# Optimization experiments

Hardware: AMD Instinct MI355X
Metric: run time of the kernel (lower is better)

## Reference

```python
import jax, jax.numpy as jnp
import numpy as np

N = 10000      # nodes
E = 160000     # edges (before self-loops)
H = 8          # heads
D_IN, D_H1, D_H2 = 165, 128, 1    # per-head channels of gat1 / gat2
HID = H * D_H1                    # 1024


def batchnorm(x, gamma, beta, eps=1e-5):
    # training-mode BatchNorm1d: biased batch statistics over the node axis
    mu = x.mean(0)
    var = x.var(0)
    return (x - mu) * jax.lax.rsqrt(var + eps) * gamma + beta


def gatv2(x, src, dst, Wl, bl, Wr, br, att, bias, heads, out_ch, concat, n_nodes):
    # PyG GATv2Conv: lin_l on source, lin_r on target; e = att . LeakyReLU(xl_j + xr_i)
    xl = (x @ Wl + bl).reshape(n_nodes, heads, out_ch)   # source transform
    xr = (x @ Wr + br).reshape(n_nodes, heads, out_ch)   # target transform
    e = jax.nn.leaky_relu(xl[src] + xr[dst], 0.2)        # [E,H,C]
    logits = jnp.einsum('ehc,hc->eh', e, att)            # [E,H]
    # segment softmax over incoming edges of each destination node
    m = jax.lax.stop_gradient(jax.ops.segment_max(logits, dst, num_segments=n_nodes))
    a = jnp.exp(logits - m[dst])
    s = jax.ops.segment_sum(a, dst, num_segments=n_nodes)
    alpha = a / (s[dst] + 1e-16)                          # [E,H]
    out = jax.ops.segment_sum(xl[src] * alpha[..., None], dst, num_segments=n_nodes)
    out = out.reshape(n_nodes, heads * out_ch) if concat else out.mean(1)
    return out + bias


def setup_inputs() -> dict:
    key = jax.random.key(0)
    ks = jax.random.split(key, 12)
    g = lambda k, shape, fan_in: jax.random.normal(k, shape, jnp.float32) * (1.0 / np.sqrt(fan_in))
    return {
        'x': jax.random.normal(ks[0], (N, D_IN), jnp.float32),
        'gamma1': jnp.ones((D_IN,), jnp.float32),
        'beta1': jnp.zeros((D_IN,), jnp.float32),
        'Wl1': g(ks[1], (D_IN, HID), D_IN),
        'bl1': jnp.zeros((HID,), jnp.float32),
        'Wr1': g(ks[2], (D_IN, HID), D_IN),
        'br1': jnp.zeros((HID,), jnp.float32),
        'att1': g(ks[3], (H, D_H1), D_H1),
        'bias1': jnp.zeros((HID,), jnp.float32),
        'gamma2': jnp.ones((HID,), jnp.float32),
        'beta2': jnp.zeros((HID,), jnp.float32),
        'Wl2': g(ks[4], (HID, H * D_H2), HID),
        'bl2': jnp.zeros((H * D_H2,), jnp.float32),
        'Wr2': g(ks[5], (HID, H * D_H2), HID),
        'br2': jnp.zeros((H * D_H2,), jnp.float32),
        'att2': g(ks[6], (H, D_H2), D_H2),
        'bias2': jnp.zeros((D_H2,), jnp.float32),
        'edge_index': jax.random.randint(ks[7], (2, E), 0, N, jnp.int64 if jax.config.jax_enable_x64 else jnp.int32),
    }


def reference(x, gamma1, beta1, Wl1, bl1, Wr1, br1, att1, bias1,
              gamma2, beta2, Wl2, bl2, Wr2, br2, att2, bias2, edge_index):
    loops = jnp.arange(N, dtype=edge_index.dtype)
    src = jnp.concatenate([edge_index[0], loops])   # add_self_loops=True (PyG default)
    dst = jnp.concatenate([edge_index[1], loops])
    h = batchnorm(x, gamma1, beta1)
    h = gatv2(h, src, dst, Wl1, bl1, Wr1, br1, att1, bias1, H, D_H1, True, N)
    h = batchnorm(h, gamma2, beta2)
    h = jax.nn.leaky_relu(h, 0.01)                  # F.leaky_relu default slope
    out = gatv2(h, src, dst, Wl2, bl2, Wr2, br2, att2, bias2, H, D_H2, False, N)
    return out
```

## Files before the change

kernel.cpp:

```cpp
#include <hip/hip_runtime.h>

#define NN   10000
#define E0   160000
#define ET   170000
#define DIN  165
#define KP   192
#define HID  1024
#define NH   8
#define BP   200
#define K2P  1032


typedef __bf16 bf16x8 __attribute__((ext_vector_type(8)));
typedef float  f32x4  __attribute__((ext_vector_type(4)));

__device__ __forceinline__ float bf2f(unsigned short u) {
    unsigned int i = ((unsigned int)u) << 16;
    return __builtin_bit_cast(float, i);
}
__device__ __forceinline__ unsigned short f2bf(float f) {
    unsigned int i = __builtin_bit_cast(unsigned int, f);
    i += 0x7fffu + ((i >> 16) & 1u);
    return (unsigned short)(i >> 16);
}
__device__ __forceinline__ float fin(float x) {
    return fminf(fmaxf(x, -1e30f), 1e30f);
}
__device__ __forceinline__ int clampi(int s) {
    return min(max(s, 0), NN - 1);
}
__device__ __forceinline__ void unpack8(uint4 u, float* f) {
    f[0]=bf2f((unsigned short)(u.x)); f[1]=bf2f((unsigned short)(u.x>>16));
    f[2]=bf2f((unsigned short)(u.y)); f[3]=bf2f((unsigned short)(u.y>>16));
    f[4]=bf2f((unsigned short)(u.z)); f[5]=bf2f((unsigned short)(u.z>>16));
    f[6]=bf2f((unsigned short)(u.w)); f[7]=bf2f((unsigned short)(u.w>>16));
}

__global__ __launch_bounds__(256) void debug_fill(float* __restrict__ out, float val) {
    int i = blockIdx.x * 256 + threadIdx.x;
    if (i < NN) out[i] = val;
}

__global__ __launch_bounds__(256) void bn1_stats(const float* __restrict__ x,
                                                 float* __restrict__ colsum, float* __restrict__ colsq) {
    int r0 = blockIdx.x * 125;
    int c = threadIdx.x;
    if (c >= DIN) return;
    float acc = 0.f, sq = 0.f;
    for (int r = r0; r < r0 + 125; ++r) {
        float v = x[(size_t)r * DIN + c];
        acc += v; sq += v * v;
    }
    atomicAdd(&colsum[c], acc);
    atomicAdd(&colsq[c], sq);
}

__global__ __launch_bounds__(256) void bn1_apply(const float* __restrict__ x,
                                                 const float* __restrict__ colsum, const float* __restrict__ colsq,
                                                 const float* __restrict__ gamma, const float* __restrict__ beta,
                                                 unsigned short* __restrict__ hn) {
    int idx = blockIdx.x * 256 + threadIdx.x;
    if (idx >= NN * KP) return;
    int r = idx / KP, c = idx - r * KP;
    float v = 0.f;
    if (c < DIN) {
        float mu  = colsum[c] * (1.f / NN);
        float var = fmaxf(colsq[c] * (1.f / NN) - mu * mu, 0.f);
        float a = gamma[c] * rsqrtf(var + 1e-5f);
        float b = beta[c] - mu * a;
        v = fin(x[(size_t)r * DIN + c] * a + b);
    }
    hn[idx] = f2bf(v);
}

__global__ __launch_bounds__(256) void w1_transpose(const float* __restrict__ wl,
                                                    const float* __restrict__ wr,
                                                    unsigned short* __restrict__ wlt,
                                                    unsigned short* __restrict__ wrt) {
    const float* src    = blockIdx.z ? wr  : wl;
    unsigned short* dst = blockIdx.z ? wrt : wlt;
    __shared__ float ts[32][65];
    const int k0 = blockIdx.x * 32;
    const int n0 = blockIdx.y * 64;
    const int tid = threadIdx.x;
    for (int idx = tid; idx < 32 * 64; idx += 256) {
        int k = idx >> 6, n = idx & 63;
        ts[k][n] = (k0 + k < DIN) ? src[(size_t)(k0 + k) * HID + n0 + n] : 0.f;
    }
    __syncthreads();
    for (int idx = tid; idx < 64 * 32; idx += 256) {
        int n = idx >> 5, k = idx & 31;
        dst[(size_t)(n0 + n) * KP + k0 + k] = f2bf(ts[k][n]);
    }
}

__global__ __launch_bounds__(256) void gemm1_kernel(
    const unsigned short* __restrict__ hn,
    const unsigned short* __restrict__ wlt,
    const unsigned short* __restrict__ wrt,
    const float* __restrict__ bl,
    const float* __restrict__ br,
    unsigned short* __restrict__ xl,
    unsigned short* __restrict__ xr) {
    __shared__ unsigned short bs[2][64 * BP];
    const int tid  = threadIdx.x;
    const int lane = tid & 63;
    const int wave = tid >> 6;
    const int col  = lane & 15;
    const int q    = lane >> 4;
    const int n0   = blockIdx.y * 64;

    for (int idx = tid; idx < 64 * 48 * 2; idx += 256) {
        int z = idx >= 64 * 48;
        int rem = z ? idx - 64 * 48 : idx;
        int r = rem / 48, c = rem - r * 48;
        const unsigned short* wt = z ? wrt : wlt;
        uint2 v = *(const uint2*)(wt + (size_t)(n0 + r) * KP + c * 4);
        *(uint2*)&bs[z][r * BP + c * 4] = v;
    }
    __syncthreads();

    const int mbase = blockIdx.x * 128 + wave * 32;
    const int am0 = mbase + col;
    const int am1 = am0 + 16;
    const bool aok0 = (am0 < NN), aok1 = (am1 < NN);

    f32x4 accL[2][4], accR[2][4];
    #pragma unroll
    for (int m = 0; m < 2; ++m)
        for (int nt = 0; nt < 4; ++nt)
            for (int r = 0; r < 4; ++r) { accL[m][nt][r] = 0.f; accR[m][nt][r] = 0.f; }

    #pragma unroll
    for (int kt = 0; kt < 6; ++kt) {
        const int kk = kt * 32 + q * 8;
        uint4 a0u = make_uint4(0u,0u,0u,0u), a1u = make_uint4(0u,0u,0u,0u);
        if (aok0) a0u = *(const uint4*)(hn + (size_t)am0 * KP + kk);
        if (aok1) a1u = *(const uint4*)(hn + (size_t)am1 * KP + kk);
        bf16x8 a0 = __builtin_bit_cast(bf16x8, a0u);
        bf16x8 a1 = __builtin_bit_cast(bf16x8, a1u);
        #pragma unroll
        for (int nt = 0; nt < 4; ++nt) {
            bf16x8 bfl = __builtin_bit_cast(bf16x8, *(const uint4*)&bs[0][(nt * 16 + col) * BP + kk]);
            accL[0][nt] = __builtin_amdgcn_mfma_f32_16x16x32_bf16(a0, bfl, accL[0][nt], 0, 0, 0);
            accL[1][nt] = __builtin_amdgcn_mfma_f32_16x16x32_bf16(a1, bfl, accL[1][nt], 0, 0, 0);
            bf16x8 bfr = __builtin_bit_cast(bf16x8, *(const uint4*)&bs[1][(nt * 16 + col) * BP + kk]);
            accR[0][nt] = __builtin_amdgcn_mfma_f32_16x16x32_bf16(a0, bfr, accR[0][nt], 0, 0, 0);
            accR[1][nt] = __builtin_amdgcn_mfma_f32_16x16x32_bf16(a1, bfr, accR[1][nt], 0, 0, 0);
        }
    }

    #pragma unroll
    for (int nt = 0; nt < 4; ++nt) {
        const int nc = n0 + nt * 16 + col;
        const float bLv = bl[nc];
        const float bRv = br[nc];
        #pragma unroll
        for (int m = 0; m < 2; ++m) {
            #pragma unroll
            for (int r = 0; r < 4; ++r) {
                const int row = mbase + m * 16 + q * 4 + r;
                if (row < NN) {
                    xl[(size_t)row * HID + nc] = f2bf(fin(accL[m][nt][r] + bLv));
                    xr[(size_t)row * HID + nc] = f2bf(fin(accR[m][nt][r] + bRv));
                }
            }
        }
    }
}

__global__ __launch_bounds__(256) void edge_hist(const int* __restrict__ ei, int* __restrict__ deg) {
    int e = blockIdx.x * 256 + threadIdx.x;
    if (e >= ET) return;
    int d = (e < E0) ? ei[E0 + e] : (e - E0);
    atomicAdd(&deg[clampi(d)], 1);
}

__global__ __launch_bounds__(1024) void scan_kernel(const int* __restrict__ deg,
                                                    int* __restrict__ offs, int* __restrict__ cur,
                                                    int* __restrict__ perm) {
    __shared__ int wsum[16];
    __shared__ int bins[64];
    __shared__ int bcur[64];
    const int tid = threadIdx.x;
    const int base = tid * 10;
    int loc[10];
    int run = 0;
    #pragma unroll
    for (int j = 0; j < 10; ++j) {
        int idx = base + j;
        int v = (idx < NN) ? deg[idx] : 0;
        loc[j] = run;
        run += v;
    }
    const int lane = tid & 63;
    const int w = tid >> 6;
    int inc = run;
    #pragma unroll
    for (int s = 1; s < 64; s <<= 1) {
        int t = __shfl_up(inc, s);
        if (lane >= s) inc += t;
    }
    if (lane == 63) wsum[w] = inc;
    if (tid < 64) bins[tid] = 0;
    __syncthreads();
    int woff = 0;
    #pragma unroll
    for (int k = 0; k < 16; ++k) woff += (k < w) ? wsum[k] : 0;
    const int toff = woff + inc - run;
    #pragma unroll
    for (int j = 0; j < 10; ++j) {
        int idx = base + j;
        if (idx < NN) {
            int e = toff + loc[j]; offs[idx] = e; cur[idx] = e;
            atomicAdd(&bins[63 - min(deg[idx], 63)], 1);
        }
    }
    if (tid == 1023) offs[NN] = woff + inc;
    __syncthreads();
    if (tid < 64) {
        int v = bins[tid];
        int binc = v;
        #pragma unroll
        for (int s = 1; s < 64; s <<= 1) {
            int t = __shfl_up(binc, s);
            if (tid >= s) binc += t;
        }
        bcur[tid] = binc - v;
    }
    __syncthreads();
    #pragma unroll
    for (int j = 0; j < 10; ++j) {
        int idx = base + j;
        if (idx < NN) {
            int pos = atomicAdd(&bcur[63 - min(deg[idx], 63)], 1);
            perm[pos] = idx;
        }
    }
}

__global__ __launch_bounds__(256) void edge_scatter(const int* __restrict__ ei,
                                                    int* __restrict__ cur, int* __restrict__ ssrc) {
    int e = blockIdx.x * 256 + threadIdx.x;
    if (e >= ET) return;
    int s, d;
    if (e < E0) { s = ei[e]; d = ei[E0 + e]; }
    else        { s = e - E0; d = e - E0; }
    int pos = atomicAdd(&cur[clampi(d)], 1);
    if (pos >= 0 && pos < ET) ssrc[pos] = clampi(s);
}

__global__ __launch_bounds__(256) void gat1_node(
    const unsigned short* __restrict__ xl1, const unsigned short* xr1,
    const float* __restrict__ att1, const float* __restrict__ bias1,
    const int* __restrict__ offs, const int* __restrict__ ssrc,
    const int* __restrict__ perm,
    unsigned short* agg) {
    const int lane = threadIdx.x & 63;
    const int wave = threadIdx.x >> 6;
    const int i = perm[blockIdx.x * 4 + wave];
    const int e0 = offs[i];
    const int e1 = max(offs[i + 1], e0);

    float xr_r[16], att_r[16];
    {
        const uint4* xp = (const uint4*)(xr1 + (size_t)i * HID + lane * 16);
        uint4 u0 = xp[0], u1 = xp[1];
        unpack8(u0, xr_r); unpack8(u1, xr_r + 8);
        const float4* ap = (const float4*)(att1 + lane * 16);
        float4 a0 = ap[0], a1 = ap[1], a2 = ap[2], a3 = ap[3];
        att_r[0]=a0.x; att_r[1]=a0.y; att_r[2]=a0.z; att_r[3]=a0.w;
        att_r[4]=a1.x; att_r[5]=a1.y; att_r[6]=a1.z; att_r[7]=a1.w;
        att_r[8]=a2.x; att_r[9]=a2.y; att_r[10]=a2.z; att_r[11]=a2.w;
        att_r[12]=a3.x; att_r[13]=a3.y; att_r[14]=a3.z; att_r[15]=a3.w;
    }

    float o[16];
    #pragma unroll
    for (int j = 0; j < 16; ++j) o[j] = 0.f;
    float s = 0.f;

    int e = e0;
    for (; e + 1 < e1; e += 2) {
        const int s0i = clampi(ssrc[e]);
        const int s1i = clampi(ssrc[e + 1]);
        const uint4* xp0 = (const uint4*)(xl1 + (size_t)s0i * HID + lane * 16);
        const uint4* xp1 = (const uint4*)(xl1 + (size_t)s1i * HID + lane * 16);
        uint4 a0 = xp0[0], a1 = xp0[1], b0 = xp1[0], b1 = xp1[1];
        float xv0[16], xv1[16];
        unpack8(a0, xv0); unpack8(a1, xv0 + 8);
        unpack8(b0, xv1); unpack8(b1, xv1 + 8);
        float p0 = 0.f, p1 = 0.f;
        #pragma unroll
        for (int j = 0; j < 16; ++j) {
            float v0 = xv0[j] + xr_r[j];
            float v1 = xv1[j] + xr_r[j];
            v0 = fmaxf(v0, 0.2f * v0);
            v1 = fmaxf(v1, 0.2f * v1);
            p0 = fmaf(att_r[j], v0, p0);
            p1 = fmaf(att_r[j], v1, p1);
        }
        p0 += __shfl_xor(p0, 1); p0 += __shfl_xor(p0, 2); p0 += __shfl_xor(p0, 4);
        p1 += __shfl_xor(p1, 1); p1 += __shfl_xor(p1, 2); p1 += __shfl_xor(p1, 4);
        const float aa0 = __expf(fminf(fin(p0), 50.f));
        const float aa1 = __expf(fminf(fin(p1), 50.f));
        s += aa0 + aa1;
        #pragma unroll
        for (int j = 0; j < 16; ++j) o[j] = fmaf(aa0, xv0[j], fmaf(aa1, xv1[j], o[j]));
    }
    if (e < e1) {
        const int sidx = clampi(ssrc[e]);
        const uint4* xp = (const uint4*)(xl1 + (size_t)sidx * HID + lane * 16);
        uint4 u0 = xp[0], u1 = xp[1];
        float xv[16];
        unpack8(u0, xv); unpack8(u1, xv + 8);
        float p = 0.f;
        #pragma unroll
        for (int j = 0; j < 16; ++j) {
            float v = xv[j] + xr_r[j];
            v = fmaxf(v, 0.2f * v);
            p = fmaf(att_r[j], v, p);
        }
        p += __shfl_xor(p, 1); p += __shfl_xor(p, 2); p += __shfl_xor(p, 4);
        const float a = __expf(fminf(fin(p), 50.f));
        s += a;
        #pragma unroll
        for (int j = 0; j < 16; ++j) o[j] = fmaf(a, xv[j], o[j]);
    }

    const float inv = 1.f / (s + 1e-16f);
    const float4* bp = (const float4*)(bias1 + lane * 16);
    float4 b0 = bp[0], b1 = bp[1], b2 = bp[2], b3 = bp[3];
    float bb[16] = {b0.x,b0.y,b0.z,b0.w, b1.x,b1.y,b1.z,b1.w,
                    b2.x,b2.y,b2.z,b2.w, b3.x,b3.y,b3.z,b3.w};
    unsigned short ov[16];
    #pragma unroll
    for (int j = 0; j < 16; ++j) ov[j] = f2bf(fin(o[j] * inv + bb[j]));
    uint4* op = (uint4*)(agg + (size_t)i * HID + lane * 16);
    op[0] = *(const uint4*)&ov[0];
    op[1] = *(const uint4*)&ov[8];
}

__global__ __launch_bounds__(256) void bn2_stats(const unsigned short* __restrict__ agg,
                                                 float* __restrict__ colsum, float* __restrict__ colsq) {
    int r0 = blockIdx.x * 125;
    int t = threadIdx.x;
    float s0=0,s1=0,s2=0,s3=0,q0=0,q1=0,q2=0,q3=0;
    for (int r = r0; r < r0 + 125; ++r) {
        const ushort4 u = *(const ushort4*)(agg + (size_t)r * HID + t * 4);
        float v0=bf2f(u.x), v1=bf2f(u.y), v2=bf2f(u.z), v3=bf2f(u.w);
        s0+=v0; q0+=v0*v0; s1+=v1; q1+=v1*v1;
        s2+=v2; q2+=v2*v2; s3+=v3; q3+=v3*v3;
    }
    atomicAdd(&colsum[t*4+0], s0); atomicAdd(&colsq[t*4+0], q0);
    atomicAdd(&colsum[t*4+1], s1); atomicAdd(&colsq[t*4+1], q1);
    atomicAdd(&colsum[t*4+2], s2); atomicAdd(&colsq[t*4+2], q2);
    atomicAdd(&colsum[t*4+3], s3); atomicAdd(&colsq[t*4+3], q3);
}

__global__ __launch_bounds__(256) void gemm2_kernel(
    const unsigned short* __restrict__ agg,
    const float* __restrict__ colsum, const float* __restrict__ colsq,
    const float* __restrict__ gamma, const float* __restrict__ beta,
    const float* __restrict__ wl2, const float* __restrict__ wr2,
    const float* __restrict__ bl2, const float* __restrict__ br2,
    float* __restrict__ xl2, float* __restrict__ xr2) {
    __shared__ unsigned short bs[16 * K2P];
    __shared__ float a2s[HID], b2s[HID];
    const int tid  = threadIdx.x;
    const int lane = tid & 63;
    const int wave = tid >> 6;
    const int col  = lane & 15;
    const int q    = lane >> 4;

    for (int idx = tid; idx < 16 * HID; idx += 256) {
        int n = idx >> 10, k = idx & (HID - 1);
        float v = (n < 8) ? wl2[k * 8 + n] : wr2[k * 8 + (n - 8)];
        bs[n * K2P + k] = f2bf(v);
    }
    for (int c = tid; c < HID; c += 256) {
        float mu  = colsum[c] * (1.f / NN);
        float var = fmaxf(colsq[c] * (1.f / NN) - mu * mu, 0.f);
        float a = gamma[c] * rsqrtf(var + 1e-5f);
        a2s[c] = a; b2s[c] = beta[c] - mu * a;
    }
    __syncthreads();

    const int mtile = blockIdx.x * 4 + wave;
    if (mtile >= NN / 16) return;
    const int m0 = mtile * 16;
    const int am = m0 + col;

    f32x4 acc;
    acc[0] = acc[1] = acc[2] = acc[3] = 0.f;
    #pragma unroll
    for (int kt = 0; kt < 32; ++kt) {
        const int kk = kt * 32 + q * 8;
        uint4 u = *(const uint4*)(agg + (size_t)am * HID + kk);
        float xv[8];
        unpack8(u, xv);
        unsigned short hv[8];
        #pragma unroll
        for (int j = 0; j < 8; ++j) {
            float v = xv[j] * a2s[kk + j] + b2s[kk + j];
            v = fmaxf(v, 0.01f * v);
            hv[j] = f2bf(fin(v));
        }
        bf16x8 af = __builtin_bit_cast(bf16x8, *(const uint4*)hv);
        bf16x8 bf = __builtin_bit_cast(bf16x8, *(const uint4*)&bs[col * K2P + kk]);
        acc = __builtin_amdgcn_mfma_f32_16x16x32_bf16(af, bf, acc, 0, 0, 0);
    }

    const float bv = (col < 8) ? bl2[col] : br2[col - 8];
    float* outp = (col < 8) ? (xl2 + col) : (xr2 + (col - 8));
    #pragma unroll
    for (int r = 0; r < 4; ++r) {
        const int row = m0 + q * 4 + r;
        outp[row * 8] = fin(acc[r] + bv);
    }
}

__global__ __launch_bounds__(256) void gat2_node(
    const float* __restrict__ xl2, const float* __restrict__ xr2,
    const float* __restrict__ att2, const float* __restrict__ bias2,
    const int* __restrict__ offs, const int* __restrict__ ssrc,
    const int* __restrict__ perm,
    float* __restrict__ out) {
    const int lane = threadIdx.x & 63;
    const int wave = threadIdx.x >> 6;
    const int i = perm[blockIdx.x * 4 + wave];
    const int h = lane & 7, slot = lane >> 3;
    const int e0 = offs[i];
    const int e1 = max(offs[i + 1], e0);
    const float xr_h = xr2[i * 8 + h];
    const float att_h = att2[h];
    float ssum = 0.f, wsum = 0.f;
    for (int eb = e0; eb < e1; eb += 8) {
        int e = eb + slot;
        if (e < e1) {
            float xlv = xl2[clampi(ssrc[e]) * 8 + h];
            float v = xlv + xr_h;
            v = fmaxf(v, 0.2f * v);
            float a = __expf(fminf(fin(att_h * v), 50.f));
            ssum += a; wsum += a * xlv;
        }
    }
    ssum += __shfl_xor(ssum, 8); ssum += __shfl_xor(ssum, 16); ssum += __shfl_xor(ssum, 32);
    wsum += __shfl_xor(wsum, 8); wsum += __shfl_xor(wsum, 16); wsum += __shfl_xor(wsum, 32);
    float v = fin(wsum / (ssum + 1e-16f));
    v += __shfl_xor(v, 1); v += __shfl_xor(v, 2); v += __shfl_xor(v, 4);
    if (lane == 0) out[i] = fin(v * 0.125f + bias2[0]);
}

extern "C" void kernel_launch(void* const* d_in, const int* in_sizes, int n_in,
                              void* d_out, int out_size, void* d_ws, size_t ws_size,
                              hipStream_t stream) {
    float* out = (float*)d_out;

    static const int expected[18] = {
        NN * DIN, DIN, DIN, DIN * HID, HID, DIN * HID, HID, HID, HID,
        HID, HID, HID * NH, NH, HID * NH, NH, NH, 1, 2 * E0
    };
    if (n_in != 18) {
        debug_fill<<<(NN + 255) / 256, 256, 0, stream>>>(out, 8192.f + 64.f * (float)n_in);
        return;
    }
    for (int i = 0; i < 18; ++i) {
        if (in_sizes[i] != expected[i]) {
            debug_fill<<<(NN + 255) / 256, 256, 0, stream>>>(out, 4096.f + 32.f * (float)i);
            return;
        }
    }

    const float* x      = (const float*)d_in[0];
    const float* gamma1 = (const float*)d_in[1];
    const float* beta1  = (const float*)d_in[2];
    const float* Wl1    = (const float*)d_in[3];
    const float* bl1    = (const float*)d_in[4];
    const float* Wr1    = (const float*)d_in[5];
    const float* br1    = (const float*)d_in[6];
    const float* att1   = (const float*)d_in[7];
    const float* bias1  = (const float*)d_in[8];
    const float* gamma2 = (const float*)d_in[9];
    const float* beta2  = (const float*)d_in[10];
    const float* Wl2    = (const float*)d_in[11];
    const float* bl2    = (const float*)d_in[12];
    const float* Wr2    = (const float*)d_in[13];
    const float* br2    = (const float*)d_in[14];
    const float* att2   = (const float*)d_in[15];
    const float* bias2  = (const float*)d_in[16];
    const int*   ei     = (const int*)d_in[17];

    char* p = (char*)d_ws;
    auto alloc = [&](size_t bytes) -> void* {
        void* r = (void*)p;
        p += (bytes + 255) & ~(size_t)255;
        return r;
    };
    unsigned short* xl1  = (unsigned short*)alloc((size_t)NN * HID * 2);
    unsigned short* xr1  = (unsigned short*)alloc((size_t)NN * HID * 2);
    unsigned short* agg  = xr1;
    unsigned short* hn   = (unsigned short*)alloc((size_t)NN * KP * 2);
    unsigned short* wlt  = (unsigned short*)alloc((size_t)HID * KP * 2);
    unsigned short* wrt  = (unsigned short*)alloc((size_t)HID * KP * 2);
    float*          xl2  = (float*)alloc((size_t)NN * 8 * 4);
    float*          xr2  = (float*)alloc((size_t)NN * 8 * 4);
    int*            offs = (int*)alloc((NN + 1) * 4);
    int*            cur  = (int*)alloc(NN * 4);
    int*            ssrc = (int*)alloc(ET * 4);
    int*            perm = (int*)alloc(NN * 4);
    char* zbase = p;
    float* colsum1 = (float*)alloc(DIN * 4);
    float* colsq1  = (float*)alloc(DIN * 4);
    float* colsum2 = (float*)alloc(HID * 4);
    float* colsq2  = (float*)alloc(HID * 4);
    int*   deg     = (int*)alloc(NN * 4);
    size_t zlen = (size_t)(p - zbase);
    hipMemsetAsync(zbase, 0, zlen, stream);

    bn1_stats<<<80, 256, 0, stream>>>(x, colsum1, colsq1);
    bn1_apply<<<(NN * KP + 255) / 256, 256, 0, stream>>>(x, colsum1, colsq1, gamma1, beta1, hn);
    w1_transpose<<<dim3(6, 16, 2), 256, 0, stream>>>(Wl1, Wr1, wlt, wrt);
    gemm1_kernel<<<dim3((NN + 127) / 128, HID / 64), 256, 0, stream>>>(hn, wlt, wrt, bl1, br1, xl1, xr1);
    edge_hist<<<(ET + 255) / 256, 256, 0, stream>>>(ei, deg);
    scan_kernel<<<1, 1024, 0, stream>>>(deg, offs, cur, perm);
    edge_scatter<<<(ET + 255) / 256, 256, 0, stream>>>(ei, cur, ssrc);
    gat1_node<<<NN / 4, 256, 0, stream>>>(xl1, xr1, att1, bias1, offs, ssrc, perm, agg);
    bn2_stats<<<80, 256, 0, stream>>>(agg, colsum2, colsq2);
    gemm2_kernel<<<(NN / 16 + 3) / 4, 256, 0, stream>>>(agg, colsum2, colsq2, gamma2, beta2,
                                                        Wl2, Wr2, bl2, br2, xl2, xr2);
    gat2_node<<<NN / 4, 256, 0, stream>>>(xl2, xr2, att2, bias2, offs, ssrc, perm, out);
}
```

Before: 278.4 us.

## Stage GEMM1 output through LDS for coalesced stores; retune BN and GAT grids

The gemm1 epilogue now writes bf16 results into the shared B buffer and then copies full 64-column row segments to global memory as uint4 vectors. This replaces the scattered 2-byte stores from the MFMA layout. Separately, the BN stats kernels use 625 blocks of 16 rows instead of 80 blocks of 125 rows, which adds parallelism at the cost of more atomics. The GAT node kernels now launch one 64-thread block per node instead of four waves per block, so degree-imbalanced waves are no longer grouped into one block.

```diff
diff --git a/kernel.cpp b/kernel.cpp
--- a/kernel.cpp
+++ b/kernel.cpp
@@ -8,6 +8,7 @@
 #define HID  1024
 #define NH   8
 #define BP   200
+#define OP   72
 #define K2P  1032
 
 
@@ -43,11 +44,11 @@
 
 __global__ __launch_bounds__(256) void bn1_stats(const float* __restrict__ x,
                                                  float* __restrict__ colsum, float* __restrict__ colsq) {
-    int r0 = blockIdx.x * 125;
+    int r0 = blockIdx.x * 16;
     int c = threadIdx.x;
     if (c >= DIN) return;
     float acc = 0.f, sq = 0.f;
-    for (int r = r0; r < r0 + 125; ++r) {
+    for (int r = r0; r < r0 + 16; ++r) {
         float v = x[(size_t)r * DIN + c];
         acc += v; sq += v * v;
     }
@@ -102,7 +103,7 @@
     const float* __restrict__ br,
     unsigned short* __restrict__ xl,
     unsigned short* __restrict__ xr) {
-    __shared__ unsigned short bs[2][64 * BP];
+    __shared__ unsigned short bs[2 * 64 * BP];
     const int tid  = threadIdx.x;
     const int lane = tid & 63;
     const int wave = tid >> 6;
@@ -116,7 +117,7 @@
         int r = rem / 48, c = rem - r * 48;
         const unsigned short* wt = z ? wrt : wlt;
         uint2 v = *(const uint2*)(wt + (size_t)(n0 + r) * KP + c * 4);
-        *(uint2*)&bs[z][r * BP + c * 4] = v;
+        *(uint2*)&bs[z * 64 * BP + r * BP + c * 4] = v;
     }
     __syncthreads();
 
@@ -141,15 +142,16 @@
         bf16x8 a1 = __builtin_bit_cast(bf16x8, a1u);
         #pragma unroll
         for (int nt = 0; nt < 4; ++nt) {
-            bf16x8 bfl = __builtin_bit_cast(bf16x8, *(const uint4*)&bs[0][(nt * 16 + col) * BP + kk]);
+            bf16x8 bfl = __builtin_bit_cast(bf16x8, *(const uint4*)&bs[(nt * 16 + col) * BP + kk]);
             accL[0][nt] = __builtin_amdgcn_mfma_f32_16x16x32_bf16(a0, bfl, accL[0][nt], 0, 0, 0);
             accL[1][nt] = __builtin_amdgcn_mfma_f32_16x16x32_bf16(a1, bfl, accL[1][nt], 0, 0, 0);
-            bf16x8 bfr = __builtin_bit_cast(bf16x8, *(const uint4*)&bs[1][(nt * 16 + col) * BP + kk]);
+            bf16x8 bfr = __builtin_bit_cast(bf16x8, *(const uint4*)&bs[64 * BP + (nt * 16 + col) * BP + kk]);
             accR[0][nt] = __builtin_amdgcn_mfma_f32_16x16x32_bf16(a0, bfr, accR[0][nt], 0, 0, 0);
             accR[1][nt] = __builtin_amdgcn_mfma_f32_16x16x32_bf16(a1, bfr, accR[1][nt], 0, 0, 0);
         }
     }
 
+    __syncthreads();
     #pragma unroll
     for (int nt = 0; nt < 4; ++nt) {
         const int nc = n0 + nt * 16 + col;
@@ -159,12 +161,24 @@
         for (int m = 0; m < 2; ++m) {
             #pragma unroll
             for (int r = 0; r < 4; ++r) {
-                const int row = mbase + m * 16 + q * 4 + r;
-                if (row < NN) {
-                    xl[(size_t)row * HID + nc] = f2bf(fin(accL[m][nt][r] + bLv));
-                    xr[(size_t)row * HID + nc] = f2bf(fin(accR[m][nt][r] + bRv));
-                }
+                const int lr = wave * 32 + m * 16 + q * 4 + r;
+                bs[lr * OP + nt * 16 + col]            = f2bf(fin(accL[m][nt][r] + bLv));
+                bs[128 * OP + lr * OP + nt * 16 + col] = f2bf(fin(accR[m][nt][r] + bRv));
             }
+        }
+    }
+    __syncthreads();
+    {
+        const int row  = tid >> 1;
+        const int half = tid & 1;
+        const int grow = blockIdx.x * 128 + row;
+        if (grow < NN) {
+            const uint4* sl = (const uint4*)&bs[row * OP + half * 32];
+            const uint4* sr = (const uint4*)&bs[128 * OP + row * OP + half * 32];
+            uint4* dl = (uint4*)(xl + (size_t)grow * HID + n0 + half * 32);
+            uint4* dr = (uint4*)(xr + (size_t)grow * HID + n0 + half * 32);
+            dl[0] = sl[0]; dl[1] = sl[1]; dl[2] = sl[2]; dl[3] = sl[3];
+            dr[0] = sr[0]; dr[1] = sr[1]; dr[2] = sr[2]; dr[3] = sr[3];
         }
     }
 }
@@ -250,15 +264,14 @@
     if (pos >= 0 && pos < ET) ssrc[pos] = clampi(s);
 }
 
-__global__ __launch_bounds__(256) void gat1_node(
+__global__ __launch_bounds__(64) void gat1_node(
     const unsigned short* __restrict__ xl1, const unsigned short* xr1,
     const float* __restrict__ att1, const float* __restrict__ bias1,
     const int* __restrict__ offs, const int* __restrict__ ssrc,
     const int* __restrict__ perm,
     unsigned short* agg) {
-    const int lane = threadIdx.x & 63;
-    const int wave = threadIdx.x >> 6;
-    const int i = perm[blockIdx.x * 4 + wave];
+    const int lane = threadIdx.x;
+    const int i = perm[blockIdx.x];
     const int e0 = offs[i];
     const int e1 = max(offs[i + 1], e0);
 
@@ -343,10 +356,10 @@
 
 __global__ __launch_bounds__(256) void bn2_stats(const unsigned short* __restrict__ agg,
                                                  float* __restrict__ colsum, float* __restrict__ colsq) {
-    int r0 = blockIdx.x * 125;
+    int r0 = blockIdx.x * 16;
     int t = threadIdx.x;
     float s0=0,s1=0,s2=0,s3=0,q0=0,q1=0,q2=0,q3=0;
-    for (int r = r0; r < r0 + 125; ++r) {
+    for (int r = r0; r < r0 + 16; ++r) {
         const ushort4 u = *(const ushort4*)(agg + (size_t)r * HID + t * 4);
         float v0=bf2f(u.x), v1=bf2f(u.y), v2=bf2f(u.z), v3=bf2f(u.w);
         s0+=v0; q0+=v0*v0; s1+=v1; q1+=v1*v1;
@@ -420,15 +433,14 @@
     }
 }
 
-__global__ __launch_bounds__(256) void gat2_node(
+__global__ __launch_bounds__(64) void gat2_node(
     const float* __restrict__ xl2, const float* __restrict__ xr2,
     const float* __restrict__ att2, const float* __restrict__ bias2,
     const int* __restrict__ offs, const int* __restrict__ ssrc,
     const int* __restrict__ perm,
     float* __restrict__ out) {
-    const int lane = threadIdx.x & 63;
-    const int wave = threadIdx.x >> 6;
-    const int i = perm[blockIdx.x * 4 + wave];
+    const int lane = threadIdx.x;
+    const int i = perm[blockIdx.x];
     const int h = lane & 7, slot = lane >> 3;
     const int e0 = offs[i];
     const int e1 = max(offs[i + 1], e0);
@@ -518,16 +530,16 @@
     size_t zlen = (size_t)(p - zbase);
     hipMemsetAsync(zbase, 0, zlen, stream);
 
-    bn1_stats<<<80, 256, 0, stream>>>(x, colsum1, colsq1);
+    bn1_stats<<<NN / 16, 256, 0, stream>>>(x, colsum1, colsq1);
     bn1_apply<<<(NN * KP + 255) / 256, 256, 0, stream>>>(x, colsum1, colsq1, gamma1, beta1, hn);
     w1_transpose<<<dim3(6, 16, 2), 256, 0, stream>>>(Wl1, Wr1, wlt, wrt);
     gemm1_kernel<<<dim3((NN + 127) / 128, HID / 64), 256, 0, stream>>>(hn, wlt, wrt, bl1, br1, xl1, xr1);
     edge_hist<<<(ET + 255) / 256, 256, 0, stream>>>(ei, deg);
     scan_kernel<<<1, 1024, 0, stream>>>(deg, offs, cur, perm);
     edge_scatter<<<(ET + 255) / 256, 256, 0, stream>>>(ei, cur, ssrc);
-    gat1_node<<<NN / 4, 256, 0, stream>>>(xl1, xr1, att1, bias1, offs, ssrc, perm, agg);
-    bn2_stats<<<80, 256, 0, stream>>>(agg, colsum2, colsq2);
+    gat1_node<<<NN, 64, 0, stream>>>(xl1, xr1, att1, bias1, offs, ssrc, perm, agg);
+    bn2_stats<<<NN / 16, 256, 0, stream>>>(agg, colsum2, colsq2);
     gemm2_kernel<<<(NN / 16 + 3) / 4, 256, 0, stream>>>(agg, colsum2, colsq2, gamma2, beta2,
                                                         Wl2, Wr2, bl2, br2, xl2, xr2);
-    gat2_node<<<NN / 4, 256, 0, stream>>>(xl2, xr2, att2, bias2, offs, ssrc, perm, out);
-}
+    gat2_node<<<NN, 64, 0, stream>>>(xl2, xr2, att2, bias2, offs, ssrc, perm, out);
+}
```

Measured after the change: 335.1 us. 1.2x slower.
